# Kernel optimization log

Hardware: AMD Instinct MI355X
Metric: run time of the kernel (lower is better)

The kernel has to match this reference:

```python
import jax, jax.numpy as jnp
import numpy as np


def setup_inputs() -> dict:
    key = jax.random.key(0)
    k1, k2 = jax.random.split(key)
    N, D = 8192, 64
    mag = jax.random.uniform(k1, (N, D), dtype=jnp.float32)
    phase = jax.random.normal(k2, (N, D), dtype=jnp.float32)
    return {"mag": mag, "phase": phase}


def reference(mag, phase):
    # score_ij = sum_d mag_i,d * mag_j,d * cos(phase_i,d - phase_j,d)
    # expanded via cos(a-b) = cos a cos b + sin a sin b into two GEMMs,
    # mathematically identical to the O(N^2 D) broadcasted form.
    a = mag * jnp.cos(phase)  # [N, D]
    b = mag * jnp.sin(phase)  # [N, D]
    scores = a @ a.T + b @ b.T  # [N, N]
    attn = jax.nn.softmax(scores, axis=1)
    new_mag = attn @ mag      # [N, D]
    new_phase = attn @ phase  # [N, D]
    return new_mag, new_phase
```

## Files before the change

### kernel.cpp

```cpp
#include <hip/hip_runtime.h>
#include <hip/hip_bf16.h>

typedef __attribute__((ext_vector_type(8))) short short8;
typedef __attribute__((ext_vector_type(4))) float f32x4;
typedef __attribute__((ext_vector_type(16))) float f32x16;
typedef __attribute__((ext_vector_type(2))) int int2v;

#define N_TOK 8192
#define D_HALF 64
#define D_FULL 128
#define QB 128
#define KQ 2048
#define CHUNK 128
#define NCH (KQ / CHUNK)
#define OSTR 132
#define RSC 1.2011224087864498f
#define MFIX 94.0f

__global__ __launch_bounds__(256) void precompute_kernel(
    const float* __restrict__ mag, const float* __restrict__ phase,
    __hip_bfloat16* __restrict__ Kf, __hip_bfloat16* __restrict__ Vf)
{
    int idx = blockIdx.x * 256 + threadIdx.x;
    if (idx >= N_TOK * D_HALF) return;
    int n = idx >> 6, d0 = idx & 63;
    float m = mag[idx], p = phase[idx];
    float s, c;
    sincosf(p, &s, &c);
    {
        float val[2] = { m * c * RSC, m * s * RSC };
        #pragma unroll
        for (int h = 0; h < 2; ++h) {
            int dc = d0 + 64 * h;
            int off = ((n >> 5) * 16 + (dc >> 4) * 2 + ((dc >> 3) & 1)) * 256
                      + (n & 31) * 8 + (dc & 7);
            Kf[off] = __float2bfloat16(val[h]);
        }
    }
    {
        float val[2] = { m, p };
        #pragma unroll
        for (int h = 0; h < 2; ++h) {
            int dv = d0 + 64 * h;
            int off = ((n >> 4) * 4 + (dv >> 5)) * 512 + ((n >> 3) & 1) * 256
                      + (dv & 31) * 8 + (n & 7);
            Vf[off] = __float2bfloat16(val[h]);
        }
    }
}

static __device__ __forceinline__ unsigned cvtpk(float a, float b)
{
    unsigned r;
    asm("v_cvt_pk_bf16_f32 %0, %1, %2" : "=v"(r) : "v"(a), "v"(b));
    return r;
}

__global__ __launch_bounds__(512, 2) void attn_kernel(
    const short8* __restrict__ Kf8, const short8* __restrict__ Vf8,
    float* __restrict__ Opart, float* __restrict__ Sp)
{
    __shared__ __align__(16) char smem[131072];

    const int tid  = threadIdx.x;
    const int wid  = tid >> 6;
    const int lane = tid & 63;
    const int li   = lane & 31;
    const int hi   = lane >> 5;
    const int qh   = wid >> 1;
    const int kp   = wid & 1;

    const int bid  = blockIdx.x;
    const int qt   = bid >> 2;
    const int kq   = bid & 3;
    const int rot  = bid & (NCH - 1);

    float (*O_lds)[32][OSTR] = (float (*)[32][OSTR])smem;
    float* s_base = (float*)(smem + 67584);
    auto sslot = [&](int slot) -> float* { return s_base + slot * 32; };

    auto stageKV = [&](int ck, char* lbase) {
        const char* gk = (const char*)(Kf8 + (size_t)ck * 2048);
        const char* gv = (const char*)(Vf8 + (size_t)ck * 2048);
        #pragma unroll
        for (int j = 0; j < 4; ++j)
            __builtin_amdgcn_global_load_lds(
                (const __attribute__((address_space(1))) void*)(gk + j * 8192 + tid * 16),
                (__attribute__((address_space(3))) void*)(lbase + j * 8192 + tid * 16),
                16, 0, 0);
        #pragma unroll
        for (int j = 0; j < 4; ++j)
            __builtin_amdgcn_global_load_lds(
                (const __attribute__((address_space(1))) void*)(gv + j * 8192 + tid * 16),
                (__attribute__((address_space(3))) void*)(lbase + 32768 + j * 8192 + tid * 16),
                16, 0, 0);
    };
    auto ck_of = [&](int t) { return kq * NCH + ((t + rot) & (NCH - 1)); };

    short8 bq[8];
    {
        const short8* qp = Kf8 + (size_t)(qt * 4 + qh) * 512;
        #pragma unroll
        for (int ks = 0; ks < 8; ++ks)
            bq[ks] = qp[(ks * 2 + hi) * 32 + li];
    }

    f32x16 acc[4];
    #pragma unroll
    for (int d = 0; d < 4; ++d) acc[d] = (f32x16)(0.0f);
    float srow = 0.0f;

    stageKV(ck_of(0), smem);
    stageKV(ck_of(1), smem + 65536);
    asm volatile("s_waitcnt vmcnt(8)");
    __builtin_amdgcn_s_barrier();

    for (int t = 0; t < NCH; ++t) {
        char* base = smem + (t & 1) * 65536;
        const short8* ldsK = (const short8*)base;
        const short8* ldsV = (const short8*)(base + 32768);

        #pragma unroll
        for (int pp = 0; pp < 2; ++pp) {
            const int panel = kp + 2 * pp;

            f32x16 st = (f32x16)(-MFIX);
            __builtin_amdgcn_s_setprio(1);
            #pragma unroll
            for (int ks = 0; ks < 8; ++ks) {
                short8 kf = ldsK[panel * 512 + (ks * 2 + hi) * 32 + li];
                st = __builtin_amdgcn_mfma_f32_32x32x16_bf16(kf, bq[ks], st, 0, 0, 0);
            }
            __builtin_amdgcn_s_setprio(0);

            #pragma unroll
            for (int r = 0; r < 16; ++r) st[r] = exp2f(st[r]);
            float sm[8];
            #pragma unroll
            for (int r = 0; r < 8; ++r) sm[r] = st[r] + st[r + 8];
            float ss = ((sm[0] + sm[1]) + (sm[2] + sm[3]))
                     + ((sm[4] + sm[5]) + (sm[6] + sm[7]));
            srow += ss + __shfl_xor(ss, 32);

            #pragma unroll
            for (int c = 0; c < 2; ++c) {
                const int b = 8 * c;
                unsigned a0 = cvtpk(st[b + 0], st[b + 1]);
                unsigned a1 = cvtpk(st[b + 2], st[b + 3]);
                unsigned b0 = cvtpk(st[b + 4], st[b + 5]);
                unsigned b1 = cvtpk(st[b + 6], st[b + 7]);
                int2v r0 = __builtin_amdgcn_permlane32_swap((int)a0, (int)b0, false, false);
                int2v r1 = __builtin_amdgcn_permlane32_swap((int)a1, (int)b1, false, false);
                union { int w[4]; short8 v; } u;
                u.w[0] = r0[0]; u.w[1] = r1[0]; u.w[2] = r0[1]; u.w[3] = r1[1];

                const short8* vp = ldsV + (panel * 2 + c) * 256 + hi * 32 + li;
                __builtin_amdgcn_s_setprio(1);
                #pragma unroll
                for (int d = 0; d < 4; ++d) {
                    short8 vf = vp[d * 64];
                    acc[d] = __builtin_amdgcn_mfma_f32_32x32x16_bf16(vf, u.v, acc[d], 0, 0, 0);
                }
                __builtin_amdgcn_s_setprio(0);
            }
        }

        __builtin_amdgcn_s_barrier();
        if (t + 2 < NCH) {
            stageKV(ck_of(t + 2), base);
            asm volatile("s_waitcnt vmcnt(8)");
        } else {
            asm volatile("s_waitcnt vmcnt(0)");
        }
        __builtin_amdgcn_s_barrier();
    }

    auto store_partial = [&](int slot) {
        #pragma unroll
        for (int d = 0; d < 4; ++d)
            #pragma unroll
            for (int rr = 0; rr < 4; ++rr) {
                f32x4 v;
                #pragma unroll
                for (int j = 0; j < 4; ++j) v[j] = acc[d][4 * rr + j];
                *reinterpret_cast<f32x4*>(&O_lds[slot][li][d * 32 + 8 * rr + 4 * hi]) = v;
            }
        if (hi == 0) sslot(slot)[li] = srow;
    };
    auto merge_partial = [&](int slot) {
        srow += sslot(slot)[li];
        #pragma unroll
        for (int d = 0; d < 4; ++d)
            #pragma unroll
            for (int rr = 0; rr < 4; ++rr) {
                f32x4 v = *reinterpret_cast<const f32x4*>(&O_lds[slot][li][d * 32 + 8 * rr + 4 * hi]);
                #pragma unroll
                for (int j = 0; j < 4; ++j)
                    acc[d][4 * rr + j] += v[j];
            }
    };

    __syncthreads();
    if (kp == 1) store_partial(qh);
    __syncthreads();
    if (kp == 0) merge_partial(qh);
    __syncthreads();
    if (kp == 0) store_partial(qh);
    __syncthreads();

    #pragma unroll
    for (int u0 = 0; u0 < 4; ++u0) {
        int u  = tid + u0 * 512;
        int q  = u >> 4;
        int dg = (u & 15) * 8;
        int grp = q >> 5, qq = q & 31;
        f32x4 o0 = *reinterpret_cast<const f32x4*>(&O_lds[grp][qq][dg]);
        f32x4 o1 = *reinterpret_cast<const f32x4*>(&O_lds[grp][qq][dg + 4]);
        size_t pidx = (size_t)bid * QB + q;
        *reinterpret_cast<f32x4*>(&Opart[pidx * D_FULL + dg])     = o0;
        *reinterpret_cast<f32x4*>(&Opart[pidx * D_FULL + dg + 4]) = o1;
        if (dg == 0) Sp[pidx] = sslot(grp)[qq];
    }
}

__global__ __launch_bounds__(256) void merge4_kernel(
    const float* __restrict__ Opart, const float* __restrict__ Sp,
    float* __restrict__ out)
{
    int i   = blockIdx.x * 256 + threadIdx.x;
    int row = i >> 5;
    int dg  = (i & 31) * 4;
    int qt  = row >> 7, qq = row & 127;
    size_t pidx[4];
    float S = 0.0f;
    #pragma unroll
    for (int k = 0; k < 4; ++k) {
        pidx[k] = (size_t)(qt * 4 + k) * QB + qq;
        S += Sp[pidx[k]];
    }
    float inv = 1.0f / S;
    f32x4 o = (f32x4)(0.0f);
    #pragma unroll
    for (int k = 0; k < 4; ++k) {
        f32x4 a = *reinterpret_cast<const f32x4*>(&Opart[pidx[k] * D_FULL + dg]);
        #pragma unroll
        for (int j = 0; j < 4; ++j) o[j] += a[j];
    }
    #pragma unroll
    for (int j = 0; j < 4; ++j) o[j] *= inv;
    float* dst = (dg < D_HALF)
        ? out + (size_t)row * D_HALF + dg
        : out + (size_t)N_TOK * D_HALF + (size_t)row * D_HALF + (dg - D_HALF);
    *reinterpret_cast<f32x4*>(dst) = o;
}

extern "C" void kernel_launch(void* const* d_in, const int* in_sizes, int n_in,
                              void* d_out, int out_size, void* d_ws, size_t ws_size,
                              hipStream_t stream)
{
    const float* mag   = (const float*)d_in[0];
    const float* phase = (const float*)d_in[1];
    float* out = (float*)d_out;

    char* ws = (char*)d_ws;
    __hip_bfloat16* Kf = (__hip_bfloat16*)ws;
    __hip_bfloat16* Vf = Kf + (size_t)N_TOK * D_FULL;
    float* Opart = (float*)(ws + 4u * 1024 * 1024);
    float* Sp    = (float*)(ws + 20u * 1024 * 1024);

    precompute_kernel<<<(N_TOK * D_HALF + 255) / 256, 256, 0, stream>>>(mag, phase, Kf, Vf);
    attn_kernel<<<256, 512, 0, stream>>>((const short8*)Kf, (const short8*)Vf, Opart, Sp);
    merge4_kernel<<<1024, 256, 0, stream>>>(Opart, Sp, out);
}
```

Before: 66.26 us.

## Halve KV chunk size and use four-slot triple-buffered prefetch pipeline

Shrinks each staged K/V chunk from 128 to 64 keys and moves from a two-slot to a four-slot LDS ring, keeping three chunks in flight. The loop is restructured so K and V fragments are loaded into registers ahead of the MFMA bursts, and the next prefetch is issued mid-iteration. The aim is to overlap global loads better and cut LDS wait stalls between the QK and PV phases. In exchange it doubles the iteration count and adds three barriers per iteration. The smem size also grows past 128KB, which may limit occupancy at two blocks per CU.

```diff
diff --git a/kernel.cpp b/kernel.cpp
--- a/kernel.cpp
+++ b/kernel.cpp
@@ -11,7 +11,7 @@
 #define D_FULL 128
 #define QB 128
 #define KQ 2048
-#define CHUNK 128
+#define CHUNK 64
 #define NCH (KQ / CHUNK)
 #define OSTR 132
 #define RSC 1.2011224087864498f
@@ -60,7 +60,7 @@
     const short8* __restrict__ Kf8, const short8* __restrict__ Vf8,
     float* __restrict__ Opart, float* __restrict__ Sp)
 {
-    __shared__ __align__(16) char smem[131072];
+    __shared__ __align__(16) char smem[132096];
 
     const int tid  = threadIdx.x;
     const int wid  = tid >> 6;
@@ -80,19 +80,19 @@
     auto sslot = [&](int slot) -> float* { return s_base + slot * 32; };
 
     auto stageKV = [&](int ck, char* lbase) {
-        const char* gk = (const char*)(Kf8 + (size_t)ck * 2048);
-        const char* gv = (const char*)(Vf8 + (size_t)ck * 2048);
-        #pragma unroll
-        for (int j = 0; j < 4; ++j)
+        const char* gk = (const char*)(Kf8 + (size_t)ck * 1024);
+        const char* gv = (const char*)(Vf8 + (size_t)ck * 1024);
+        #pragma unroll
+        for (int j = 0; j < 2; ++j)
             __builtin_amdgcn_global_load_lds(
                 (const __attribute__((address_space(1))) void*)(gk + j * 8192 + tid * 16),
                 (__attribute__((address_space(3))) void*)(lbase + j * 8192 + tid * 16),
                 16, 0, 0);
         #pragma unroll
-        for (int j = 0; j < 4; ++j)
+        for (int j = 0; j < 2; ++j)
             __builtin_amdgcn_global_load_lds(
                 (const __attribute__((address_space(1))) void*)(gv + j * 8192 + tid * 16),
-                (__attribute__((address_space(3))) void*)(lbase + 32768 + j * 8192 + tid * 16),
+                (__attribute__((address_space(3))) void*)(lbase + 16384 + j * 8192 + tid * 16),
                 16, 0, 0);
     };
     auto ck_of = [&](int t) { return kq * NCH + ((t + rot) & (NCH - 1)); };
@@ -111,67 +111,76 @@
     float srow = 0.0f;
 
     stageKV(ck_of(0), smem);
-    stageKV(ck_of(1), smem + 65536);
+    stageKV(ck_of(1), smem + 32768);
+    stageKV(ck_of(2), smem + 65536);
     asm volatile("s_waitcnt vmcnt(8)");
     __builtin_amdgcn_s_barrier();
 
     for (int t = 0; t < NCH; ++t) {
-        char* base = smem + (t & 1) * 65536;
-        const short8* ldsK = (const short8*)base;
-        const short8* ldsV = (const short8*)(base + 32768);
-
-        #pragma unroll
-        for (int pp = 0; pp < 2; ++pp) {
-            const int panel = kp + 2 * pp;
-
-            f32x16 st = (f32x16)(-MFIX);
-            __builtin_amdgcn_s_setprio(1);
-            #pragma unroll
-            for (int ks = 0; ks < 8; ++ks) {
-                short8 kf = ldsK[panel * 512 + (ks * 2 + hi) * 32 + li];
-                st = __builtin_amdgcn_mfma_f32_32x32x16_bf16(kf, bq[ks], st, 0, 0, 0);
-            }
-            __builtin_amdgcn_s_setprio(0);
-
-            #pragma unroll
-            for (int r = 0; r < 16; ++r) st[r] = exp2f(st[r]);
-            float sm[8];
-            #pragma unroll
-            for (int r = 0; r < 8; ++r) sm[r] = st[r] + st[r + 8];
-            float ss = ((sm[0] + sm[1]) + (sm[2] + sm[3]))
-                     + ((sm[4] + sm[5]) + (sm[6] + sm[7]));
-            srow += ss + __shfl_xor(ss, 32);
-
-            #pragma unroll
-            for (int c = 0; c < 2; ++c) {
-                const int b = 8 * c;
-                unsigned a0 = cvtpk(st[b + 0], st[b + 1]);
-                unsigned a1 = cvtpk(st[b + 2], st[b + 3]);
-                unsigned b0 = cvtpk(st[b + 4], st[b + 5]);
-                unsigned b1 = cvtpk(st[b + 6], st[b + 7]);
-                int2v r0 = __builtin_amdgcn_permlane32_swap((int)a0, (int)b0, false, false);
-                int2v r1 = __builtin_amdgcn_permlane32_swap((int)a1, (int)b1, false, false);
-                union { int w[4]; short8 v; } u;
-                u.w[0] = r0[0]; u.w[1] = r1[0]; u.w[2] = r0[1]; u.w[3] = r1[1];
-
-                const short8* vp = ldsV + (panel * 2 + c) * 256 + hi * 32 + li;
-                __builtin_amdgcn_s_setprio(1);
-                #pragma unroll
-                for (int d = 0; d < 4; ++d) {
-                    short8 vf = vp[d * 64];
-                    acc[d] = __builtin_amdgcn_mfma_f32_32x32x16_bf16(vf, u.v, acc[d], 0, 0, 0);
-                }
-                __builtin_amdgcn_s_setprio(0);
-            }
+        char* base = smem + (size_t)(t & 3) * 32768;
+        const short8* bK = (const short8*)base;
+        const short8* bV = (const short8*)(base + 16384);
+
+        short8 kfr[8];
+        #pragma unroll
+        for (int ks = 0; ks < 8; ++ks)
+            kfr[ks] = bK[kp * 512 + (ks * 2 + hi) * 32 + li];
+        __builtin_amdgcn_s_barrier();
+        asm volatile("s_waitcnt lgkmcnt(0)" ::: "memory");
+        __builtin_amdgcn_sched_barrier(0);
+        f32x16 st = (f32x16)(-MFIX);
+        __builtin_amdgcn_s_setprio(1);
+        #pragma unroll
+        for (int ks = 0; ks < 8; ++ks)
+            st = __builtin_amdgcn_mfma_f32_32x32x16_bf16(kfr[ks], bq[ks], st, 0, 0, 0);
+        __builtin_amdgcn_s_setprio(0);
+        __builtin_amdgcn_s_barrier();
+
+        short8 vfr[8];
+        #pragma unroll
+        for (int c = 0; c < 2; ++c)
+            #pragma unroll
+            for (int d = 0; d < 4; ++d)
+                vfr[c * 4 + d] = bV[((kp * 2 + c) * 4 + d) * 64 + hi * 32 + li];
+        if (t + 3 < NCH)
+            stageKV(ck_of(t + 3), smem + (size_t)((t + 3) & 3) * 32768);
+        __builtin_amdgcn_s_barrier();
+
+        #pragma unroll
+        for (int r = 0; r < 16; ++r) st[r] = exp2f(st[r]);
+        float sm[8];
+        #pragma unroll
+        for (int r = 0; r < 8; ++r) sm[r] = st[r] + st[r + 8];
+        float ss = ((sm[0] + sm[1]) + (sm[2] + sm[3]))
+                 + ((sm[4] + sm[5]) + (sm[6] + sm[7]));
+        srow += ss + __shfl_xor(ss, 32);
+
+        union { int w[4]; short8 v; } u[2];
+        #pragma unroll
+        for (int c = 0; c < 2; ++c) {
+            const int b = 8 * c;
+            unsigned a0 = cvtpk(st[b + 0], st[b + 1]);
+            unsigned a1 = cvtpk(st[b + 2], st[b + 3]);
+            unsigned b0 = cvtpk(st[b + 4], st[b + 5]);
+            unsigned b1 = cvtpk(st[b + 6], st[b + 7]);
+            int2v r0 = __builtin_amdgcn_permlane32_swap((int)a0, (int)b0, false, false);
+            int2v r1 = __builtin_amdgcn_permlane32_swap((int)a1, (int)b1, false, false);
+            u[c].w[0] = r0[0]; u[c].w[1] = r1[0]; u[c].w[2] = r0[1]; u[c].w[3] = r1[1];
         }
 
-        __builtin_amdgcn_s_barrier();
-        if (t + 2 < NCH) {
-            stageKV(ck_of(t + 2), base);
-            asm volatile("s_waitcnt vmcnt(8)");
-        } else {
-            asm volatile("s_waitcnt vmcnt(0)");
-        }
+        asm volatile("s_waitcnt lgkmcnt(0)" ::: "memory");
+        __builtin_amdgcn_sched_barrier(0);
+        __builtin_amdgcn_s_setprio(1);
+        #pragma unroll
+        for (int c = 0; c < 2; ++c)
+            #pragma unroll
+            for (int d = 0; d < 4; ++d)
+                acc[d] = __builtin_amdgcn_mfma_f32_32x32x16_bf16(vfr[c * 4 + d], u[c].v, acc[d], 0, 0, 0);
+        __builtin_amdgcn_s_setprio(0);
+
+        if (t + 3 < NCH)      asm volatile("s_waitcnt vmcnt(8)");
+        else if (t + 2 < NCH) asm volatile("s_waitcnt vmcnt(4)");
+        else                  asm volatile("s_waitcnt vmcnt(0)");
         __builtin_amdgcn_s_barrier();
     }
 
```

Result: slower. 68.94 us (+4.0%).

## Have each wave process two query tiles and one key panel

Applied to the files above, without the earlier changes.

The work split inside the attention block changes from 4 query groups x 2 key panels to 2 query groups x 4 key panels. Each wave now holds two 32-row query tiles and reuses each loaded K and V fragment across two MFMAs, which halves LDS reads per MFMA. The cost is doubled accumulator register pressure (two sets of 4 f32x16 accumulators plus two bq arrays), which may spill or lower occupancy under launch_bounds(512,2). The epilogue now does a two-level reduction across four key-panel waves, run once per query tile, with extra barriers.

```diff
diff --git a/kernel.cpp b/kernel.cpp
--- a/kernel.cpp
+++ b/kernel.cpp
@@ -60,15 +60,15 @@
     const short8* __restrict__ Kf8, const short8* __restrict__ Vf8,
     float* __restrict__ Opart, float* __restrict__ Sp)
 {
-    __shared__ __align__(16) char smem[131072];
+    __shared__ __align__(16) char smem[132096];
 
     const int tid  = threadIdx.x;
     const int wid  = tid >> 6;
     const int lane = tid & 63;
     const int li   = lane & 31;
     const int hi   = lane >> 5;
-    const int qh   = wid >> 1;
-    const int kp   = wid & 1;
+    const int qh   = wid >> 2;
+    const int kp   = wid & 3;
 
     const int bid  = blockIdx.x;
     const int qt   = bid >> 2;
@@ -97,18 +97,21 @@
     };
     auto ck_of = [&](int t) { return kq * NCH + ((t + rot) & (NCH - 1)); };
 
-    short8 bq[8];
-    {
-        const short8* qp = Kf8 + (size_t)(qt * 4 + qh) * 512;
+    short8 bq[2][8];
+    #pragma unroll
+    for (int j = 0; j < 2; ++j) {
+        const short8* qp = Kf8 + (size_t)(qt * 4 + qh * 2 + j) * 512;
         #pragma unroll
         for (int ks = 0; ks < 8; ++ks)
-            bq[ks] = qp[(ks * 2 + hi) * 32 + li];
-    }
-
-    f32x16 acc[4];
-    #pragma unroll
-    for (int d = 0; d < 4; ++d) acc[d] = (f32x16)(0.0f);
-    float srow = 0.0f;
+            bq[j][ks] = qp[(ks * 2 + hi) * 32 + li];
+    }
+
+    f32x16 acc[2][4];
+    #pragma unroll
+    for (int j = 0; j < 2; ++j)
+        #pragma unroll
+        for (int d = 0; d < 4; ++d) acc[j][d] = (f32x16)(0.0f);
+    float srow[2] = { 0.0f, 0.0f };
 
     stageKV(ck_of(0), smem);
     stageKV(ck_of(1), smem + 65536);
@@ -117,53 +120,73 @@
 
     for (int t = 0; t < NCH; ++t) {
         char* base = smem + (t & 1) * 65536;
-        const short8* ldsK = (const short8*)base;
-        const short8* ldsV = (const short8*)(base + 32768);
-
-        #pragma unroll
-        for (int pp = 0; pp < 2; ++pp) {
-            const int panel = kp + 2 * pp;
-
-            f32x16 st = (f32x16)(-MFIX);
-            __builtin_amdgcn_s_setprio(1);
-            #pragma unroll
-            for (int ks = 0; ks < 8; ++ks) {
-                short8 kf = ldsK[panel * 512 + (ks * 2 + hi) * 32 + li];
-                st = __builtin_amdgcn_mfma_f32_32x32x16_bf16(kf, bq[ks], st, 0, 0, 0);
-            }
-            __builtin_amdgcn_s_setprio(0);
-
-            #pragma unroll
-            for (int r = 0; r < 16; ++r) st[r] = exp2f(st[r]);
+        const short8* bK = (const short8*)base;
+        const short8* bV = (const short8*)(base + 32768);
+
+        f32x16 st0 = (f32x16)(-MFIX), st1 = (f32x16)(-MFIX);
+        __builtin_amdgcn_s_setprio(1);
+        #pragma unroll
+        for (int ks = 0; ks < 8; ++ks) {
+            short8 kf = bK[kp * 512 + (ks * 2 + hi) * 32 + li];
+            st0 = __builtin_amdgcn_mfma_f32_32x32x16_bf16(kf, bq[0][ks], st0, 0, 0, 0);
+            st1 = __builtin_amdgcn_mfma_f32_32x32x16_bf16(kf, bq[1][ks], st1, 0, 0, 0);
+        }
+        __builtin_amdgcn_s_setprio(0);
+
+        union { int w[4]; short8 v; } u0[2], u1[2];
+        {
+            #pragma unroll
+            for (int r = 0; r < 16; ++r) st0[r] = exp2f(st0[r]);
             float sm[8];
             #pragma unroll
-            for (int r = 0; r < 8; ++r) sm[r] = st[r] + st[r + 8];
+            for (int r = 0; r < 8; ++r) sm[r] = st0[r] + st0[r + 8];
             float ss = ((sm[0] + sm[1]) + (sm[2] + sm[3]))
                      + ((sm[4] + sm[5]) + (sm[6] + sm[7]));
-            srow += ss + __shfl_xor(ss, 32);
-
+            srow[0] += ss + __shfl_xor(ss, 32);
             #pragma unroll
             for (int c = 0; c < 2; ++c) {
                 const int b = 8 * c;
-                unsigned a0 = cvtpk(st[b + 0], st[b + 1]);
-                unsigned a1 = cvtpk(st[b + 2], st[b + 3]);
-                unsigned b0 = cvtpk(st[b + 4], st[b + 5]);
-                unsigned b1 = cvtpk(st[b + 6], st[b + 7]);
-                int2v r0 = __builtin_amdgcn_permlane32_swap((int)a0, (int)b0, false, false);
-                int2v r1 = __builtin_amdgcn_permlane32_swap((int)a1, (int)b1, false, false);
-                union { int w[4]; short8 v; } u;
-                u.w[0] = r0[0]; u.w[1] = r1[0]; u.w[2] = r0[1]; u.w[3] = r1[1];
-
-                const short8* vp = ldsV + (panel * 2 + c) * 256 + hi * 32 + li;
-                __builtin_amdgcn_s_setprio(1);
-                #pragma unroll
-                for (int d = 0; d < 4; ++d) {
-                    short8 vf = vp[d * 64];
-                    acc[d] = __builtin_amdgcn_mfma_f32_32x32x16_bf16(vf, u.v, acc[d], 0, 0, 0);
-                }
-                __builtin_amdgcn_s_setprio(0);
+                unsigned a0 = cvtpk(st0[b + 0], st0[b + 1]);
+                unsigned a1 = cvtpk(st0[b + 2], st0[b + 3]);
+                unsigned c0 = cvtpk(st0[b + 4], st0[b + 5]);
+                unsigned c1 = cvtpk(st0[b + 6], st0[b + 7]);
+                int2v r0 = __builtin_amdgcn_permlane32_swap((int)a0, (int)c0, false, false);
+                int2v r1 = __builtin_amdgcn_permlane32_swap((int)a1, (int)c1, false, false);
+                u0[c].w[0] = r0[0]; u0[c].w[1] = r1[0]; u0[c].w[2] = r0[1]; u0[c].w[3] = r1[1];
             }
         }
+        {
+            #pragma unroll
+            for (int r = 0; r < 16; ++r) st1[r] = exp2f(st1[r]);
+            float sm[8];
+            #pragma unroll
+            for (int r = 0; r < 8; ++r) sm[r] = st1[r] + st1[r + 8];
+            float ss = ((sm[0] + sm[1]) + (sm[2] + sm[3]))
+                     + ((sm[4] + sm[5]) + (sm[6] + sm[7]));
+            srow[1] += ss + __shfl_xor(ss, 32);
+            #pragma unroll
+            for (int c = 0; c < 2; ++c) {
+                const int b = 8 * c;
+                unsigned a0 = cvtpk(st1[b + 0], st1[b + 1]);
+                unsigned a1 = cvtpk(st1[b + 2], st1[b + 3]);
+                unsigned c0 = cvtpk(st1[b + 4], st1[b + 5]);
+                unsigned c1 = cvtpk(st1[b + 6], st1[b + 7]);
+                int2v r0 = __builtin_amdgcn_permlane32_swap((int)a0, (int)c0, false, false);
+                int2v r1 = __builtin_amdgcn_permlane32_swap((int)a1, (int)c1, false, false);
+                u1[c].w[0] = r0[0]; u1[c].w[1] = r1[0]; u1[c].w[2] = r0[1]; u1[c].w[3] = r1[1];
+            }
+        }
+
+        __builtin_amdgcn_s_setprio(1);
+        #pragma unroll
+        for (int c = 0; c < 2; ++c)
+            #pragma unroll
+            for (int d = 0; d < 4; ++d) {
+                short8 vf = bV[((kp * 2 + c) * 4 + d) * 64 + hi * 32 + li];
+                acc[0][d] = __builtin_amdgcn_mfma_f32_32x32x16_bf16(vf, u0[c].v, acc[0][d], 0, 0, 0);
+                acc[1][d] = __builtin_amdgcn_mfma_f32_32x32x16_bf16(vf, u1[c].v, acc[1][d], 0, 0, 0);
+            }
+        __builtin_amdgcn_s_setprio(0);
 
         __builtin_amdgcn_s_barrier();
         if (t + 2 < NCH) {
@@ -175,51 +198,60 @@
         __builtin_amdgcn_s_barrier();
     }
 
-    auto store_partial = [&](int slot) {
-        #pragma unroll
-        for (int d = 0; d < 4; ++d)
-            #pragma unroll
-            for (int rr = 0; rr < 4; ++rr) {
-                f32x4 v;
+    __syncthreads();
+    #pragma unroll
+    for (int j = 0; j < 2; ++j) {
+        auto store_partial = [&](int slot) {
+            #pragma unroll
+            for (int d = 0; d < 4; ++d)
                 #pragma unroll
-                for (int j = 0; j < 4; ++j) v[j] = acc[d][4 * rr + j];
-                *reinterpret_cast<f32x4*>(&O_lds[slot][li][d * 32 + 8 * rr + 4 * hi]) = v;
-            }
-        if (hi == 0) sslot(slot)[li] = srow;
-    };
-    auto merge_partial = [&](int slot) {
-        srow += sslot(slot)[li];
-        #pragma unroll
-        for (int d = 0; d < 4; ++d)
-            #pragma unroll
-            for (int rr = 0; rr < 4; ++rr) {
-                f32x4 v = *reinterpret_cast<const f32x4*>(&O_lds[slot][li][d * 32 + 8 * rr + 4 * hi]);
+                for (int rr = 0; rr < 4; ++rr) {
+                    f32x4 v;
+                    #pragma unroll
+                    for (int jj = 0; jj < 4; ++jj) v[jj] = acc[j][d][4 * rr + jj];
+                    *reinterpret_cast<f32x4*>(&O_lds[slot][li][d * 32 + 8 * rr + 4 * hi]) = v;
+                }
+            if (hi == 0) sslot(slot)[li] = srow[j];
+        };
+        auto merge_partial = [&](int slot) {
+            srow[j] += sslot(slot)[li];
+            #pragma unroll
+            for (int d = 0; d < 4; ++d)
                 #pragma unroll
-                for (int j = 0; j < 4; ++j)
-                    acc[d][4 * rr + j] += v[j];
-            }
-    };
-
-    __syncthreads();
-    if (kp == 1) store_partial(qh);
-    __syncthreads();
-    if (kp == 0) merge_partial(qh);
-    __syncthreads();
-    if (kp == 0) store_partial(qh);
-    __syncthreads();
-
-    #pragma unroll
-    for (int u0 = 0; u0 < 4; ++u0) {
-        int u  = tid + u0 * 512;
-        int q  = u >> 4;
-        int dg = (u & 15) * 8;
-        int grp = q >> 5, qq = q & 31;
-        f32x4 o0 = *reinterpret_cast<const f32x4*>(&O_lds[grp][qq][dg]);
-        f32x4 o1 = *reinterpret_cast<const f32x4*>(&O_lds[grp][qq][dg + 4]);
-        size_t pidx = (size_t)bid * QB + q;
-        *reinterpret_cast<f32x4*>(&Opart[pidx * D_FULL + dg])     = o0;
-        *reinterpret_cast<f32x4*>(&Opart[pidx * D_FULL + dg + 4]) = o1;
-        if (dg == 0) Sp[pidx] = sslot(grp)[qq];
+                for (int rr = 0; rr < 4; ++rr) {
+                    f32x4 v = *reinterpret_cast<const f32x4*>(&O_lds[slot][li][d * 32 + 8 * rr + 4 * hi]);
+                    #pragma unroll
+                    for (int jj = 0; jj < 4; ++jj)
+                        acc[j][d][4 * rr + jj] += v[jj];
+                }
+        };
+
+        if (kp >= 2) store_partial(qh * 2 + (kp - 2));
+        __syncthreads();
+        if (kp < 2) merge_partial(qh * 2 + kp);
+        __syncthreads();
+        if (kp == 1) store_partial(qh);
+        __syncthreads();
+        if (kp == 0) merge_partial(qh);
+        __syncthreads();
+        if (kp == 0) store_partial(qh);
+        __syncthreads();
+
+        #pragma unroll
+        for (int u0i = 0; u0i < 2; ++u0i) {
+            int u  = tid + u0i * 512;
+            int q64 = u >> 4;
+            int dg  = (u & 15) * 8;
+            int grp = q64 >> 5, qq = q64 & 31;
+            int qglob = (grp * 2 + j) * 32 + qq;
+            f32x4 o0 = *reinterpret_cast<const f32x4*>(&O_lds[grp][qq][dg]);
+            f32x4 o1 = *reinterpret_cast<const f32x4*>(&O_lds[grp][qq][dg + 4]);
+            size_t pidx = (size_t)bid * QB + qglob;
+            *reinterpret_cast<f32x4*>(&Opart[pidx * D_FULL + dg])     = o0;
+            *reinterpret_cast<f32x4*>(&Opart[pidx * D_FULL + dg + 4]) = o1;
+            if (dg == 0) Sp[pidx] = sslot(grp)[qq];
+        }
+        __syncthreads();
     }
 }
 
@@ -244,10 +276,10 @@
     for (int k = 0; k < 4; ++k) {
         f32x4 a = *reinterpret_cast<const f32x4*>(&Opart[pidx[k] * D_FULL + dg]);
         #pragma unroll
-        for (int j = 0; j < 4; ++j) o[j] += a[j];
-    }
-    #pragma unroll
-    for (int j = 0; j < 4; ++j) o[j] *= inv;
+        for (int jj = 0; jj < 4; ++jj) o[jj] += a[jj];
+    }
+    #pragma unroll
+    for (int jj = 0; jj < 4; ++jj) o[jj] *= inv;
     float* dst = (dg < D_HALF)
         ? out + (size_t)row * D_HALF + dg
         : out + (size_t)N_TOK * D_HALF + (size_t)row * D_HALF + (dg - D_HALF);
```

Measured after the change: 78.10 us. 17.9% more time.
